# Kernel optimization log

Measured on AMD Instinct MI355X. Metric: run time of the kernel, lower is better.

Reference implementation:

```python
import jax, jax.numpy as jnp
import numpy as np


def setup_inputs() -> dict:
    key = jax.random.key(0)
    ks = jax.random.split(key, 7)
    B, T, I, H, O = 64, 2048, 32, 256, 32
    s = 0.05
    return {
        "x": jax.random.normal(ks[0], (B, T, I), dtype=jnp.float32),
        "W_ih": jax.random.normal(ks[1], (4 * H, I), dtype=jnp.float32) * s,
        "W_hh": jax.random.normal(ks[2], (4 * H, H), dtype=jnp.float32) * s,
        "b_ih": jax.random.normal(ks[3], (4 * H,), dtype=jnp.float32) * s,
        "b_hh": jax.random.normal(ks[4], (4 * H,), dtype=jnp.float32) * s,
        "fc_w": jax.random.normal(ks[5], (O, H), dtype=jnp.float32) * s,
        "fc_b": jax.random.normal(ks[6], (O,), dtype=jnp.float32) * s,
    }


def _lstm(x, W_ih, W_hh, b_ih, b_hh):
    # x: [B,T,I]; PyTorch gate order: i, f, g, o stacked along 4H axis.
    B = x.shape[0]
    H = W_hh.shape[1]
    # Precompute input contributions for all timesteps in one GEMM: [B,T,4H]
    xg = jnp.einsum('bti,gi->btg', x, W_ih) + b_ih + b_hh

    def step(carry, xg_t):
        h, c = carry  # [B,H] each
        gates = xg_t + h @ W_hh.T  # [B,4H]
        i, f, g, o = jnp.split(gates, 4, axis=-1)
        i = jax.nn.sigmoid(i)
        f = jax.nn.sigmoid(f)
        g = jnp.tanh(g)
        o = jax.nn.sigmoid(o)
        c = f * c + i * g
        h = o * jnp.tanh(c)
        return (h, c), h

    h0 = jnp.zeros((B, H), dtype=x.dtype)
    (_, _), hs = jax.lax.scan(step, (h0, h0), jnp.swapaxes(xg, 0, 1))
    return jnp.swapaxes(hs, 0, 1)  # [B,T,H]


def reference(x, W_ih, W_hh, b_ih, b_hh, fc_w, fc_b):
    out = _lstm(x, W_ih, W_hh, b_ih, b_hh)          # [B,T,H]
    # Conv1d(H, O, kernel_size=1) over channel dim == pointwise linear.
    return jnp.einsum('bth,oh->bto', out, fc_w) + fc_b  # [B,T,O]
```

## Files before the change

kernel.cpp:

```cpp
#include <hip/hip_runtime.h>
#include <cstdint>


#define B_  64
#define T_  2048
#define I_  32
#define H_  256
#define G4  1024
#define O_  32

typedef int v16i __attribute__((ext_vector_type(16)));
typedef int v4i  __attribute__((ext_vector_type(4)));
typedef _Float16 h2_t __attribute__((ext_vector_type(2)));

#if __has_builtin(__builtin_amdgcn_sdot4)
__device__ __forceinline__ int dot4(int a, int b, int c) {
    return __builtin_amdgcn_sdot4(a, b, c, false);
}
#else
__device__ __forceinline__ int dot4(int a, int b, int c) {
    c += (int)(int8_t)(a)        * (int)(int8_t)(b);
    c += (int)(int8_t)(a >> 8)   * (int)(int8_t)(b >> 8);
    c += (int)(int8_t)(a >> 16)  * (int)(int8_t)(b >> 16);
    c += (int)(int8_t)(a >> 24)  * (int)(int8_t)(b >> 24);
    return c;
}
#endif

__device__ __forceinline__ float fdot2h(h2_t a, h2_t b, float c) {
#if __has_builtin(__builtin_amdgcn_fdot2)
    return __builtin_amdgcn_fdot2(a, b, c, false);
#else
    return c + (float)a[0] * (float)b[0] + (float)a[1] * (float)b[1];
#endif
}

#define QWHH_OFF 0u
#define QWIH_OFF 262144u
#define S1_OFF   294912u
#define S2_OFF   299008u
#define BIAS_OFF 303104u
#define XQ_OFF   307200u
#define HBUF_OFF 9744384u
#define XREC  72
#define HREC  512
#define HSLOTS 2049

__device__ __forceinline__ uint32_t pack_q(int q0, int q1, int q2, int q3) {
    return  ((uint32_t)(uint8_t)(int8_t)q0)
          | (((uint32_t)(uint8_t)(int8_t)q1) << 8)
          | (((uint32_t)(uint8_t)(int8_t)q2) << 16)
          | (((uint32_t)(uint8_t)(int8_t)q3) << 24);
}
__device__ __forceinline__ int clamp127(int v) {
    return v < -127 ? -127 : (v > 127 ? 127 : v);
}

__global__ __launch_bounds__(64) void prep_w(
    const float* __restrict__ Whh, const float* __restrict__ Wih,
    const float* __restrict__ bih, const float* __restrict__ bhh,
    uint32_t* __restrict__ qwhh, uint32_t* __restrict__ qwih,
    float* __restrict__ s1, float* __restrict__ s2, float* __restrict__ bias)
{
    const int r = blockIdx.x;
    const int l = threadIdx.x;

    const float4 wv = ((const float4*)(Whh + r * H_))[l];
    float m = fmaxf(fmaxf(fabsf(wv.x), fabsf(wv.y)), fmaxf(fabsf(wv.z), fabsf(wv.w)));
    #pragma unroll
    for (int s = 1; s < 64; s <<= 1) m = fmaxf(m, __shfl_xor(m, s, 64));
    const float S1 = fmaxf(m, 1e-20f) / 127.f;

    float xm = (l < I_) ? fabsf(Wih[r * I_ + l]) : 0.f;
    #pragma unroll
    for (int s = 1; s < 64; s <<= 1) xm = fmaxf(xm, __shfl_xor(xm, s, 64));
    const float S2 = fmaxf(xm, 1e-20f) / 127.f;

    {
        const float r1 = 1.f / S1;
        qwhh[l * G4 + r] = pack_q(
            clamp127((int)rintf(wv.x * r1)), clamp127((int)rintf(wv.y * r1)),
            clamp127((int)rintf(wv.z * r1)), clamp127((int)rintf(wv.w * r1)));
    }
    if (l < 8) {
        const float4 xw = ((const float4*)(Wih + r * I_))[l];
        const float r2 = 1.f / S2;
        qwih[l * G4 + r] = pack_q(
            clamp127((int)rintf(xw.x * r2)), clamp127((int)rintf(xw.y * r2)),
            clamp127((int)rintf(xw.z * r2)), clamp127((int)rintf(xw.w * r2)));
    }
    if (l == 0) { s1[r] = S1; s2[r] = S2; bias[r] = bih[r] + bhh[r]; }
}

__global__ __launch_bounds__(256) void prep_x(
    const float* __restrict__ x, char* __restrict__ xq)
{
    __shared__ float xb[64 * 32];
    const int base = blockIdx.x * 64 * 32;
    for (int i = threadIdx.x; i < 2048; i += 256) xb[i] = x[base + i];
    __syncthreads();
    const int t = threadIdx.x;
    if (t < 64) {
        float m = 0.f;
        for (int k = 0; k < 32; k++) m = fmaxf(m, fabsf(xb[t * 32 + k]));
        const float S = fmaxf(m, 1e-20f) / 127.f;
        const float rS = 1.f / S;
        const int row = blockIdx.x * 64 + t;
        uint32_t* rec = (uint32_t*)(xq + (size_t)row * XREC);
        for (int jj = 0; jj < 8; jj++) {
            int qa[4], qb[4];
            for (int e = 0; e < 4; e++) {
                float v = xb[t * 32 + jj * 4 + e] * rS;
                int a = clamp127((int)rintf(v));
                int b = clamp127((int)rintf((v - (float)a) * 127.f));
                qa[e] = a; qb[e] = b;
            }
            rec[jj]     = pack_q(qa[0], qa[1], qa[2], qa[3]);
            rec[8 + jj] = pack_q(qb[0], qb[1], qb[2], qb[3]);
        }
        ((float*)rec)[16] = S;
    }
}

#define GRP16(GACC, WOFF, HV, SC) { int a_ = 0; \
    a_ = dot4((int)w[(WOFF)+0],  HV[0],  a_); \
    a_ = dot4((int)w[(WOFF)+1],  HV[1],  a_); \
    a_ = dot4((int)w[(WOFF)+2],  HV[2],  a_); \
    a_ = dot4((int)w[(WOFF)+3],  HV[3],  a_); \
    a_ = dot4((int)w[(WOFF)+4],  HV[4],  a_); \
    a_ = dot4((int)w[(WOFF)+5],  HV[5],  a_); \
    a_ = dot4((int)w[(WOFF)+6],  HV[6],  a_); \
    a_ = dot4((int)w[(WOFF)+7],  HV[7],  a_); \
    a_ = dot4((int)w[(WOFF)+8],  HV[8],  a_); \
    a_ = dot4((int)w[(WOFF)+9],  HV[9],  a_); \
    a_ = dot4((int)w[(WOFF)+10], HV[10], a_); \
    a_ = dot4((int)w[(WOFF)+11], HV[11], a_); \
    a_ = dot4((int)w[(WOFF)+12], HV[12], a_); \
    a_ = dot4((int)w[(WOFF)+13], HV[13], a_); \
    a_ = dot4((int)w[(WOFF)+14], HV[14], a_); \
    a_ = dot4((int)w[(WOFF)+15], HV[15], a_); \
    GACC = fmaf((float)a_, (SC), GACC); }

__global__ __launch_bounds__(1024, 4) void lstm_main(
    const uint32_t* __restrict__ qwhh, const uint32_t* __restrict__ qwih,
    const float* __restrict__ s1v, const float* __restrict__ s2v,
    const float* __restrict__ biasv, const char* __restrict__ xq,
    char* __restrict__ hbuf)
{
    const int b   = blockIdx.x;
    const int tid = threadIdx.x;
    const int w_  = tid >> 6, l = tid & 63;
    const int g   = w_ >> 2;
    const int u   = tid & 255;

    __shared__ float gbuf[1024];

    uint32_t w[64];
    #pragma unroll
    for (int d = 0; d < 64; d++) w[d] = qwhh[d * G4 + tid];
    uint32_t wx[8];
    #pragma unroll
    for (int k = 0; k < 8; k++) wx[k] = qwih[k * G4 + tid];

    const float S1 = s1v[tid], S2 = s2v[tid], biasr = biasv[tid];
    const float sA = (g == 2) ? 2.f : 1.f;
    const float mA = (g == 2) ? 2.f : 1.f;
    const float cA = (g == 2) ? -1.f : 0.f;

    char* hb = hbuf + (size_t)b * ((size_t)HSLOTS * HREC);
    const char* xb = xq + (size_t)b * T_ * XREC;
    if (tid < 68) ((uint32_t*)hb)[tid] = 0u;
    float c_state = 0.f;
    __syncthreads();

    for (int t = 0; t < T_; t++) {
        const char* hrec = hb + (size_t)t * HREC;
        const char* xrec = xb + (size_t)t * XREC;
        v16i h0, h1, h2, h3, xv; v4i scv; int sxi;
        asm volatile(
            "s_load_dwordx16 %0, %7, 0x0\n\t"
            "s_load_dwordx16 %1, %7, 0x40\n\t"
            "s_load_dwordx16 %2, %7, 0x80\n\t"
            "s_load_dwordx16 %3, %7, 0xc0\n\t"
            "s_load_dwordx4  %4, %7, 0x100\n\t"
            "s_load_dwordx16 %5, %8, 0x0\n\t"
            "s_load_dword    %6, %8, 0x40\n\t"
            "s_waitcnt lgkmcnt(0)"
            : "=&s"(h0), "=&s"(h1), "=&s"(h2), "=&s"(h3), "=&s"(scv),
              "=&s"(xv), "=&s"(sxi)
            : "s"(hrec), "s"(xrec)
            : "memory");

        float gacc = 0.f;
        GRP16(gacc,  0, h0, __int_as_float(scv[0]));
        GRP16(gacc, 16, h1, __int_as_float(scv[1]));
        GRP16(gacc, 32, h2, __int_as_float(scv[2]));
        GRP16(gacc, 48, h3, __int_as_float(scv[3]));

        int aA = 0, aL = 0;
        #pragma unroll
        for (int k = 0; k < 8; k++) {
            aA = dot4((int)wx[k], xv[k],     aA);
            aL = dot4((int)wx[k], xv[8 + k], aL);
        }
        const float Sx = __int_as_float(sxi);
        const float xc = ((float)aA + (float)aL * (1.f / 127.f)) * (S2 * Sx) + biasr;

        const float gate = gacc * S1 + xc;
        const float y = fmaf(1.f / (1.f + __expf(-sA * gate)), mA, cA);

        if (g > 0) gbuf[(g << 8) | u] = y;
        __syncthreads();

        char* hw = hb + (size_t)(t + 1) * HREC;
        if (g == 0) {
            const float yf = gbuf[256 + tid];
            const float yg = gbuf[512 + tid];
            const float yo = gbuf[768 + tid];
            c_state = yf * c_state + y * yg;
            const float tc = 2.f / (1.f + __expf(-2.f * c_state)) - 1.f;
            const float hval = yo * tc;

            float m = fabsf(hval);
            #pragma unroll
            for (int s = 1; s < 64; s <<= 1) m = fmaxf(m, __shfl_xor(m, s, 64));
            m = fmaxf(m, 1e-12f);
            const int q = clamp127((int)rintf(hval * (127.f / m)));

            uint32_t q8 = (uint32_t)q & 0xffu;
            uint32_t p = q8 | (((uint32_t)__shfl_xor((int)q8, 1, 64)) << 8);
            p = p | (((uint32_t)__shfl_xor((int)p, 2, 64)) << 16);
            if ((l & 3) == 0) *(uint32_t*)(hw + tid) = p;
            if (l == 0) ((float*)(hw + 256))[w_] = m * (1.f / 127.f);
        }
        __syncthreads();
    }
}

__global__ __launch_bounds__(256) void fc_kernel(
    const char* __restrict__ hbuf, const float* __restrict__ fcw,
    const float* __restrict__ fcb, float* __restrict__ out)
{
    __shared__ uint32_t hlds[64 * 128];
    __shared__ uint32_t wlds[32 * 32 * 4];
    const int b  = blockIdx.x >> 5;
    const int t0 = (blockIdx.x & 31) * 64;
    const char* hb = hbuf + (size_t)b * ((size_t)HSLOTS * HREC);

    {
        const int rec = threadIdx.x >> 2, g4 = threadIdx.x & 3;
        const char* rp = hb + (size_t)(t0 + rec + 1) * HREC;
        const float sc = *(const float*)(rp + 256 + 4 * g4);
        #pragma unroll
        for (int qq = 0; qq < 4; qq++) {
            const uint4 d = *(const uint4*)(rp + 64 * g4 + 16 * qq);
            uint32_t vals[4] = {d.x, d.y, d.z, d.w};
            #pragma unroll
            for (int e = 0; e < 4; e++) {
                const uint32_t v = vals[e];
                union { h2_t h; uint32_t u; } p0, p1;
                p0.h[0] = (_Float16)((float)(int)(int8_t)(v)       * sc);
                p0.h[1] = (_Float16)((float)(int)(int8_t)(v >> 8)  * sc);
                p1.h[0] = (_Float16)((float)(int)(int8_t)(v >> 16) * sc);
                p1.h[1] = (_Float16)((float)(int)(int8_t)(v >> 24) * sc);
                const int di = rec * 128 + g4 * 32 + qq * 8 + e * 2;
                hlds[di]     = p0.u;
                hlds[di + 1] = p1.u;
            }
        }
    }
    for (int i = threadIdx.x; i < 4096; i += 256) {
        const int o = i >> 7, kp = i & 127;
        union { h2_t h; uint32_t u; } cv;
        cv.h[0] = (_Float16)fcw[o * 256 + 2 * kp];
        cv.h[1] = (_Float16)fcw[o * 256 + 2 * kp + 1];
        wlds[((kp >> 2) * 32 + o) * 4 + (kp & 3)] = cv.u;
    }
    __syncthreads();

    const int o = threadIdx.x & 31, rg = threadIdx.x >> 5;
    const float bv = fcb[o];
    float acc[8];
    #pragma unroll
    for (int rr = 0; rr < 8; rr++) acc[rr] = bv;

    for (int ch = 0; ch < 32; ch++) {
        const uint4 wv = *(const uint4*)(wlds + (ch * 32 + o) * 4);
        union { uint32_t u; h2_t h; } w0, w1, w2, w3;
        w0.u = wv.x; w1.u = wv.y; w2.u = wv.z; w3.u = wv.w;
        #pragma unroll
        for (int rr = 0; rr < 8; rr++) {
            const int rowi = rg * 8 + rr;
            const uint4 hv = *(const uint4*)(hlds + rowi * 128 + ch * 4);
            union { uint32_t u; h2_t h; } x0, x1, x2, x3;
            x0.u = hv.x; x1.u = hv.y; x2.u = hv.z; x3.u = hv.w;
            float a = acc[rr];
            a = fdot2h(w0.h, x0.h, a);
            a = fdot2h(w1.h, x1.h, a);
            a = fdot2h(w2.h, x2.h, a);
            a = fdot2h(w3.h, x3.h, a);
            acc[rr] = a;
        }
    }
    #pragma unroll
    for (int rr = 0; rr < 8; rr++)
        out[((size_t)b * T_ + t0 + rg * 8 + rr) * O_ + o] = acc[rr];
}

extern "C" void kernel_launch(void* const* d_in, const int* in_sizes, int n_in,
                              void* d_out, int out_size, void* d_ws, size_t ws_size,
                              hipStream_t stream) {
    const float* x    = (const float*)d_in[0];
    const float* Wih  = (const float*)d_in[1];
    const float* Whh  = (const float*)d_in[2];
    const float* bih  = (const float*)d_in[3];
    const float* bhh  = (const float*)d_in[4];
    const float* fcw  = (const float*)d_in[5];
    const float* fcb  = (const float*)d_in[6];
    float* out = (float*)d_out;

    char* ws = (char*)d_ws;
    uint32_t* qwhh = (uint32_t*)(ws + QWHH_OFF);
    uint32_t* qwih = (uint32_t*)(ws + QWIH_OFF);
    float*    s1   = (float*)(ws + S1_OFF);
    float*    s2   = (float*)(ws + S2_OFF);
    float*    bias = (float*)(ws + BIAS_OFF);
    char*     xq   = ws + XQ_OFF;
    char*     hbuf = ws + HBUF_OFF;

    prep_w<<<G4, 64, 0, stream>>>(Whh, Wih, bih, bhh, qwhh, qwih, s1, s2, bias);
    prep_x<<<(B_ * T_) / 64, 256, 0, stream>>>(x, xq);
    lstm_main<<<B_, 1024, 0, stream>>>(qwhh, qwih, s1, s2, bias, xq, hbuf);
    fc_kernel<<<(B_ * T_) / 64, 256, 0, stream>>>(hbuf, fcw, fcb, out);
}
```

Before: 3.686 ms.

## Interleave gate columns per wavefront to replace LDS gate exchange with shuffles

Weight columns are permuted so each wavefront holds all four gates (i,f,g,o) for 16 hidden units, letting the cell update gather gate values via cross-lane shuffles instead of an LDS buffer and an extra block barrier per timestep. The h quantization now uses 16 per-group scales instead of 4, which changes the record layout that the FC kernel reads. The x record is prefetched into vector registers one step ahead, and the input-projection dot products are computed while the scalar h loads are in flight. Only 16 of 64 lanes per wave do the cell update, and the finer quantization groups change numerics slightly.

```diff
diff --git a/kernel.cpp b/kernel.cpp
--- a/kernel.cpp
+++ b/kernel.cpp
@@ -10,7 +10,6 @@
 #define O_  32
 
 typedef int v16i __attribute__((ext_vector_type(16)));
-typedef int v4i  __attribute__((ext_vector_type(4)));
 typedef _Float16 h2_t __attribute__((ext_vector_type(2)));
 
 #if __has_builtin(__builtin_amdgcn_sdot4)
@@ -56,6 +55,7 @@
     return v < -127 ? -127 : (v > 127 ? 127 : v);
 }
 
+
 __global__ __launch_bounds__(64) void prep_w(
     const float* __restrict__ Whh, const float* __restrict__ Wih,
     const float* __restrict__ bih, const float* __restrict__ bhh,
@@ -64,6 +64,8 @@
 {
     const int r = blockIdx.x;
     const int l = threadIdx.x;
+    const int u = r & 255, g = r >> 8;
+    const int col = ((u >> 4) << 6) + (g << 4) + (u & 15);
 
     const float4 wv = ((const float4*)(Whh + r * H_))[l];
     float m = fmaxf(fmaxf(fabsf(wv.x), fabsf(wv.y)), fmaxf(fabsf(wv.z), fabsf(wv.w)));
@@ -78,18 +80,18 @@
 
     {
         const float r1 = 1.f / S1;
-        qwhh[l * G4 + r] = pack_q(
+        qwhh[l * G4 + col] = pack_q(
             clamp127((int)rintf(wv.x * r1)), clamp127((int)rintf(wv.y * r1)),
             clamp127((int)rintf(wv.z * r1)), clamp127((int)rintf(wv.w * r1)));
     }
     if (l < 8) {
         const float4 xw = ((const float4*)(Wih + r * I_))[l];
         const float r2 = 1.f / S2;
-        qwih[l * G4 + r] = pack_q(
+        qwih[l * G4 + col] = pack_q(
             clamp127((int)rintf(xw.x * r2)), clamp127((int)rintf(xw.y * r2)),
             clamp127((int)rintf(xw.z * r2)), clamp127((int)rintf(xw.w * r2)));
     }
-    if (l == 0) { s1[r] = S1; s2[r] = S2; bias[r] = bih[r] + bhh[r]; }
+    if (l == 0) { s1[col] = S1; s2[col] = S2; bias[col] = bih[r] + bhh[r]; }
 }
 
 __global__ __launch_bounds__(256) void prep_x(
@@ -122,23 +124,11 @@
     }
 }
 
-#define GRP16(GACC, WOFF, HV, SC) { int a_ = 0; \
-    a_ = dot4((int)w[(WOFF)+0],  HV[0],  a_); \
-    a_ = dot4((int)w[(WOFF)+1],  HV[1],  a_); \
-    a_ = dot4((int)w[(WOFF)+2],  HV[2],  a_); \
-    a_ = dot4((int)w[(WOFF)+3],  HV[3],  a_); \
-    a_ = dot4((int)w[(WOFF)+4],  HV[4],  a_); \
-    a_ = dot4((int)w[(WOFF)+5],  HV[5],  a_); \
-    a_ = dot4((int)w[(WOFF)+6],  HV[6],  a_); \
-    a_ = dot4((int)w[(WOFF)+7],  HV[7],  a_); \
-    a_ = dot4((int)w[(WOFF)+8],  HV[8],  a_); \
-    a_ = dot4((int)w[(WOFF)+9],  HV[9],  a_); \
-    a_ = dot4((int)w[(WOFF)+10], HV[10], a_); \
-    a_ = dot4((int)w[(WOFF)+11], HV[11], a_); \
-    a_ = dot4((int)w[(WOFF)+12], HV[12], a_); \
-    a_ = dot4((int)w[(WOFF)+13], HV[13], a_); \
-    a_ = dot4((int)w[(WOFF)+14], HV[14], a_); \
-    a_ = dot4((int)w[(WOFF)+15], HV[15], a_); \
+#define GRP4(GACC, HV, D0, SC) { int a_ = 0; \
+    a_ = dot4((int)w[(D0)+0], HV[((D0)+0) & 15], a_); \
+    a_ = dot4((int)w[(D0)+1], HV[((D0)+1) & 15], a_); \
+    a_ = dot4((int)w[(D0)+2], HV[((D0)+2) & 15], a_); \
+    a_ = dot4((int)w[(D0)+3], HV[((D0)+3) & 15], a_); \
     GACC = fmaf((float)a_, (SC), GACC); }
 
 __global__ __launch_bounds__(1024, 4) void lstm_main(
@@ -150,10 +140,7 @@
     const int b   = blockIdx.x;
     const int tid = threadIdx.x;
     const int w_  = tid >> 6, l = tid & 63;
-    const int g   = w_ >> 2;
-    const int u   = tid & 255;
-
-    __shared__ float gbuf[1024];
+    const int g   = l >> 4;
 
     uint32_t w[64];
     #pragma unroll
@@ -164,73 +151,99 @@
 
     const float S1 = s1v[tid], S2 = s2v[tid], biasr = biasv[tid];
     const float sA = (g == 2) ? 2.f : 1.f;
-    const float mA = (g == 2) ? 2.f : 1.f;
+    const float mA = sA;
     const float cA = (g == 2) ? -1.f : 0.f;
 
     char* hb = hbuf + (size_t)b * ((size_t)HSLOTS * HREC);
-    const char* xb = xq + (size_t)b * T_ * XREC;
-    if (tid < 68) ((uint32_t*)hb)[tid] = 0u;
+    const char* xbp = xq + (size_t)b * T_ * XREC;
+    if (tid < 80) ((uint32_t*)hb)[tid] = 0u;
     float c_state = 0.f;
+
+    uint4 x0v, x1v, x2v, x3v; float Sx;
+    {
+        const uint4* xr = (const uint4*)xbp;
+        x0v = xr[0]; x1v = xr[1]; x2v = xr[2]; x3v = xr[3];
+        Sx = *(const float*)(xbp + 64);
+    }
     __syncthreads();
 
     for (int t = 0; t < T_; t++) {
         const char* hrec = hb + (size_t)t * HREC;
-        const char* xrec = xb + (size_t)t * XREC;
-        v16i h0, h1, h2, h3, xv; v4i scv; int sxi;
+        v16i h0, h1, h2, h3, scv;
         asm volatile(
-            "s_load_dwordx16 %0, %7, 0x0\n\t"
-            "s_load_dwordx16 %1, %7, 0x40\n\t"
-            "s_load_dwordx16 %2, %7, 0x80\n\t"
-            "s_load_dwordx16 %3, %7, 0xc0\n\t"
-            "s_load_dwordx4  %4, %7, 0x100\n\t"
-            "s_load_dwordx16 %5, %8, 0x0\n\t"
-            "s_load_dword    %6, %8, 0x40\n\t"
-            "s_waitcnt lgkmcnt(0)"
-            : "=&s"(h0), "=&s"(h1), "=&s"(h2), "=&s"(h3), "=&s"(scv),
-              "=&s"(xv), "=&s"(sxi)
-            : "s"(hrec), "s"(xrec)
+            "s_load_dwordx16 %0, %5, 0x0\n\t"
+            "s_load_dwordx16 %1, %5, 0x40\n\t"
+            "s_load_dwordx16 %2, %5, 0x80\n\t"
+            "s_load_dwordx16 %3, %5, 0xc0\n\t"
+            "s_load_dwordx16 %4, %5, 0x100"
+            : "=&s"(h0), "=&s"(h1), "=&s"(h2), "=&s"(h3), "=&s"(scv)
+            : "s"(hrec)
             : "memory");
 
+        int aA = 0, aL = 0;
+        aA = dot4((int)wx[0], (int)x0v.x, aA); aA = dot4((int)wx[1], (int)x0v.y, aA);
+        aA = dot4((int)wx[2], (int)x0v.z, aA); aA = dot4((int)wx[3], (int)x0v.w, aA);
+        aA = dot4((int)wx[4], (int)x1v.x, aA); aA = dot4((int)wx[5], (int)x1v.y, aA);
+        aA = dot4((int)wx[6], (int)x1v.z, aA); aA = dot4((int)wx[7], (int)x1v.w, aA);
+        aL = dot4((int)wx[0], (int)x2v.x, aL); aL = dot4((int)wx[1], (int)x2v.y, aL);
+        aL = dot4((int)wx[2], (int)x2v.z, aL); aL = dot4((int)wx[3], (int)x2v.w, aL);
+        aL = dot4((int)wx[4], (int)x3v.x, aL); aL = dot4((int)wx[5], (int)x3v.y, aL);
+        aL = dot4((int)wx[6], (int)x3v.z, aL); aL = dot4((int)wx[7], (int)x3v.w, aL);
+        const float xcontrib =
+            ((float)aA + (float)aL * (1.f / 127.f)) * (S2 * Sx) + biasr;
+
+        asm volatile("s_waitcnt lgkmcnt(0)"
+                     : "+s"(h0), "+s"(h1), "+s"(h2), "+s"(h3), "+s"(scv));
+
         float gacc = 0.f;
-        GRP16(gacc,  0, h0, __int_as_float(scv[0]));
-        GRP16(gacc, 16, h1, __int_as_float(scv[1]));
-        GRP16(gacc, 32, h2, __int_as_float(scv[2]));
-        GRP16(gacc, 48, h3, __int_as_float(scv[3]));
-
-        int aA = 0, aL = 0;
-        #pragma unroll
-        for (int k = 0; k < 8; k++) {
-            aA = dot4((int)wx[k], xv[k],     aA);
-            aL = dot4((int)wx[k], xv[8 + k], aL);
-        }
-        const float Sx = __int_as_float(sxi);
-        const float xc = ((float)aA + (float)aL * (1.f / 127.f)) * (S2 * Sx) + biasr;
-
-        const float gate = gacc * S1 + xc;
+        GRP4(gacc, h0,  0, __int_as_float(scv[0]));
+        GRP4(gacc, h0,  4, __int_as_float(scv[1]));
+        GRP4(gacc, h0,  8, __int_as_float(scv[2]));
+        GRP4(gacc, h0, 12, __int_as_float(scv[3]));
+        GRP4(gacc, h1, 16, __int_as_float(scv[4]));
+        GRP4(gacc, h1, 20, __int_as_float(scv[5]));
+        GRP4(gacc, h1, 24, __int_as_float(scv[6]));
+        GRP4(gacc, h1, 28, __int_as_float(scv[7]));
+        GRP4(gacc, h2, 32, __int_as_float(scv[8]));
+        GRP4(gacc, h2, 36, __int_as_float(scv[9]));
+        GRP4(gacc, h2, 40, __int_as_float(scv[10]));
+        GRP4(gacc, h2, 44, __int_as_float(scv[11]));
+        GRP4(gacc, h3, 48, __int_as_float(scv[12]));
+        GRP4(gacc, h3, 52, __int_as_float(scv[13]));
+        GRP4(gacc, h3, 56, __int_as_float(scv[14]));
+        GRP4(gacc, h3, 60, __int_as_float(scv[15]));
+
+        const float gate = gacc * S1 + xcontrib;
         const float y = fmaf(1.f / (1.f + __expf(-sA * gate)), mA, cA);
 
-        if (g > 0) gbuf[(g << 8) | u] = y;
-        __syncthreads();
+        const float yf = __shfl_xor(y, 16, 64);
+        const float yg = __shfl_xor(y, 32, 64);
+        const float yo = __shfl_xor(y, 48, 64);
+
+        {
+            const uint4* xr = (const uint4*)(xbp + (size_t)(t + 1) * XREC);
+            x0v = xr[0]; x1v = xr[1]; x2v = xr[2]; x3v = xr[3];
+            Sx = *(const float*)(xbp + (size_t)(t + 1) * XREC + 64);
+        }
 
         char* hw = hb + (size_t)(t + 1) * HREC;
-        if (g == 0) {
-            const float yf = gbuf[256 + tid];
-            const float yg = gbuf[512 + tid];
-            const float yo = gbuf[768 + tid];
+        if (l < 16) {
             c_state = yf * c_state + y * yg;
             const float tc = 2.f / (1.f + __expf(-2.f * c_state)) - 1.f;
             const float hval = yo * tc;
 
             float m = fabsf(hval);
-            #pragma unroll
-            for (int s = 1; s < 64; s <<= 1) m = fmaxf(m, __shfl_xor(m, s, 64));
+            m = fmaxf(m, __shfl_xor(m, 1, 64));
+            m = fmaxf(m, __shfl_xor(m, 2, 64));
+            m = fmaxf(m, __shfl_xor(m, 4, 64));
+            m = fmaxf(m, __shfl_xor(m, 8, 64));
             m = fmaxf(m, 1e-12f);
             const int q = clamp127((int)rintf(hval * (127.f / m)));
 
             uint32_t q8 = (uint32_t)q & 0xffu;
             uint32_t p = q8 | (((uint32_t)__shfl_xor((int)q8, 1, 64)) << 8);
             p = p | (((uint32_t)__shfl_xor((int)p, 2, 64)) << 16);
-            if ((l & 3) == 0) *(uint32_t*)(hw + tid) = p;
+            if ((l & 3) == 0) *(uint32_t*)(hw + 16 * w_ + l) = p;
             if (l == 0) ((float*)(hw + 256))[w_] = m * (1.f / 127.f);
         }
         __syncthreads();
@@ -250,9 +263,9 @@
     {
         const int rec = threadIdx.x >> 2, g4 = threadIdx.x & 3;
         const char* rp = hb + (size_t)(t0 + rec + 1) * HREC;
-        const float sc = *(const float*)(rp + 256 + 4 * g4);
         #pragma unroll
         for (int qq = 0; qq < 4; qq++) {
+            const float sc = *(const float*)(rp + 256 + 4 * (g4 * 4 + qq));
             const uint4 d = *(const uint4*)(rp + 64 * g4 + 16 * qq);
             uint32_t vals[4] = {d.x, d.y, d.z, d.w};
             #pragma unroll
@@ -292,13 +305,13 @@
         for (int rr = 0; rr < 8; rr++) {
             const int rowi = rg * 8 + rr;
             const uint4 hv = *(const uint4*)(hlds + rowi * 128 + ch * 4);
-            union { uint32_t u; h2_t h; } x0, x1, x2, x3;
-            x0.u = hv.x; x1.u = hv.y; x2.u = hv.z; x3.u = hv.w;
+            union { uint32_t u; h2_t h; } y0, y1, y2, y3;
+            y0.u = hv.x; y1.u = hv.y; y2.u = hv.z; y3.u = hv.w;
             float a = acc[rr];
-            a = fdot2h(w0.h, x0.h, a);
-            a = fdot2h(w1.h, x1.h, a);
-            a = fdot2h(w2.h, x2.h, a);
-            a = fdot2h(w3.h, x3.h, a);
+            a = fdot2h(w0.h, y0.h, a);
+            a = fdot2h(w1.h, y1.h, a);
+            a = fdot2h(w2.h, y2.h, a);
+            a = fdot2h(w3.h, y3.h, a);
             acc[rr] = a;
         }
     }
```

New measurement: 4.377 ms. +18.7%, slower.
